# Performance work log

Measured on AMD Instinct MI355X. Metric: run time of the kernel, lower is better.

Reference implementation:

```python
import jax, jax.numpy as jnp
import numpy as np

B, D, N = 512, 512, 196  # batch, hidden dim, kb elements (14x14 feature grid)


def setup_inputs() -> dict:
    key = jax.random.key(0)
    ks = jax.random.split(key, 8)
    s = 1.0 / np.sqrt(D)
    return {
        "memory_state": jax.random.normal(ks[0], (B, D), jnp.float32),
        "knowledge_base": jax.random.normal(ks[1], (B, D, N), jnp.float32),
        "ctrl_state": jax.random.normal(ks[2], (B, D), jnp.float32),
        "kb_proj": jax.random.normal(ks[3], (B, D, N), jnp.float32),
        "W_mem": jax.random.normal(ks[4], (D, D), jnp.float32) * s,
        "b_mem": jnp.zeros((D,), jnp.float32),
        "W_cat": jax.random.normal(ks[5], (D, 2 * D), jnp.float32) * s,
        "b_cat": jnp.zeros((D,), jnp.float32),
        "W_attn": jax.random.normal(ks[6], (1, D), jnp.float32) * s,
        "b_attn": jnp.zeros((1,), jnp.float32),
    }


def reference(memory_state, knowledge_base, ctrl_state, kb_proj,
              W_mem, b_mem, W_cat, b_cat, W_attn, b_attn):
    # mem projection: [B, D]
    mem = memory_state @ W_mem.T + b_mem
    # interaction with projected knowledge base: [B, D, N]
    I_elements = mem[:, :, None] * kb_proj
    # concat along channel dim -> [B, 2D, N], permute to [B, N, 2D]
    cat = jnp.concatenate([I_elements, knowledge_base], axis=1).transpose(0, 2, 1)
    # concat layer: [B, N, D]
    concat = cat @ W_cat.T + b_cat
    # gate by control state, attention logits: [B, N]
    rai = ((concat * ctrl_state[:, None, :]) @ W_attn.T + b_attn)[:, :, 0]
    rvi = jax.nn.softmax(rai, axis=1)  # [B, N]
    # weighted sum over kb elements: [B, D]
    read_vector = jnp.einsum('bn,bdn->bd', rvi, knowledge_base)
    return read_vector
```

## Files before the change

kernel.cpp:

```cpp
#include <hip/hip_runtime.h>
#include <hip/hip_bf16.h>


constexpr int D = 512;
constexpr int N = 196;
constexpr int NF4 = 49;

using f4 = __attribute__((ext_vector_type(4))) float;

__global__ __launch_bounds__(256) void phase_a(
    const float* __restrict__ ms, const float* __restrict__ ctrl,
    const float* __restrict__ Wmem, const float* __restrict__ bmem,
    const float* __restrict__ Wcat, const float* __restrict__ Wattn,
    float* __restrict__ mem_ws, float* __restrict__ v_ws)
{
    constexpr int PAD = 68;
    __shared__ float As[16 * PAD];
    __shared__ float Bs[16 * PAD];

    const int bid = blockIdx.x;
    const int t   = threadIdx.x;
    const int tx  = t & 15, ty = t >> 4;

    const bool g1 = (bid < 64);
    int tile_m, tile_n;
    if (g1) { tile_m = (bid >> 3) * 64; tile_n = (bid & 7) * 64; }
    else    { int bb = bid - 64; tile_m = (bb >> 4) * 64; tile_n = (bb & 15) * 64; }

    float acc[4][4] = {};

    for (int k0 = 0; k0 < 512; k0 += 16) {
        {
            const int k = t & 15;
            const int mbase = t >> 4;
#pragma unroll
            for (int r = 0; r < 4; r++) {
                const int m = mbase + 16 * r;
                const int row = tile_m + m;
                float a;
                if (g1) a = ms[row * 512 + k0 + k];
                else    a = ctrl[row * 512 + k0 + k] * Wattn[k0 + k];
                As[k * PAD + m] = a;
            }
        }
        if (g1) {
            const int k = t & 15;
            const int nbase = t >> 4;
#pragma unroll
            for (int r = 0; r < 4; r++) {
                const int n = nbase + 16 * r;
                Bs[k * PAD + n] = Wmem[(tile_n + n) * 512 + k0 + k];
            }
        } else {
            const int n = t & 63;
            const int kbase = t >> 6;
#pragma unroll
            for (int r = 0; r < 4; r++) {
                const int k = kbase + 4 * r;
                Bs[k * PAD + n] = Wcat[(k0 + k) * 1024 + tile_n + n];
            }
        }
        __syncthreads();
#pragma unroll
        for (int k = 0; k < 16; k++) {
            const float4 av = *reinterpret_cast<const float4*>(&As[k * PAD + ty * 4]);
            const float4 bv = *reinterpret_cast<const float4*>(&Bs[k * PAD + tx * 4]);
            const float a[4] = {av.x, av.y, av.z, av.w};
            const float bb[4] = {bv.x, bv.y, bv.z, bv.w};
#pragma unroll
            for (int i = 0; i < 4; i++)
#pragma unroll
                for (int j = 0; j < 4; j++)
                    acc[i][j] += a[i] * bb[j];
        }
        __syncthreads();
    }

    if (g1) {
#pragma unroll
        for (int i = 0; i < 4; i++) {
            const int row = tile_m + ty * 4 + i;
#pragma unroll
            for (int j = 0; j < 4; j++) {
                const int col = tile_n + tx * 4 + j;
                mem_ws[row * 512 + col] = acc[i][j] + bmem[col];
            }
        }
    } else {
#pragma unroll
        for (int i = 0; i < 4; i++) {
            const int row = tile_m + ty * 4 + i;
#pragma unroll
            for (int j = 0; j < 4; j++) {
                const int col = tile_n + tx * 4 + j;
                v_ws[row * 1024 + col] = acc[i][j];
            }
        }
    }
}

__global__ __launch_bounds__(256) void k_rai(
    const f4* __restrict__ kb, const f4* __restrict__ kbp,
    const float* __restrict__ mem_ws, const float* __restrict__ v_ws,
    float* __restrict__ rai_ws)
{
    __shared__ float p_s[256];
    __shared__ float q_s[256];
    __shared__ float part[4][200];

    const int bid = blockIdx.x;
    const int b   = bid >> 1;
    const int s   = bid & 1;
    const int d0  = s * 256;
    const int t    = threadIdx.x;
    const int lane = t & 63;
    const int w    = t >> 6;

    {
        const int d = d0 + t;
        p_s[t] = mem_ws[b * D + d] * v_ws[b * 2 * D + d];
        q_s[t] = v_ws[b * 2 * D + D + d];
    }
    __syncthreads();

    const int lc = (lane < NF4) ? lane : (NF4 - 1);
    const f4* kb_b  = kb  + (size_t)b * (D * NF4);
    const f4* kbp_b = kbp + (size_t)b * (D * NF4);

    float a0 = 0.f, a1 = 0.f, a2 = 0.f, a3 = 0.f;
    const int dw = d0 + w * 64;
#pragma unroll 4
    for (int r = 0; r < 64; r++) {
        const int d = dw + r;
        const f4 vp = __builtin_nontemporal_load(&kbp_b[(size_t)d * NF4 + lc]);
        const f4 vk = kb_b[(size_t)d * NF4 + lc];
        const float pd = p_s[d - d0];
        const float qd = q_s[d - d0];
        a0 += pd * vp.x + qd * vk.x;
        a1 += pd * vp.y + qd * vk.y;
        a2 += pd * vp.z + qd * vk.z;
        a3 += pd * vp.w + qd * vk.w;
    }

    if (lane < NF4) {
        part[w][4 * lane + 0] = a0;
        part[w][4 * lane + 1] = a1;
        part[w][4 * lane + 2] = a2;
        part[w][4 * lane + 3] = a3;
    }
    __syncthreads();

    if (t < N) {
        const float r = part[0][t] + part[1][t] + part[2][t] + part[3][t];
        rai_ws[(size_t)(b * 2 + s) * N + t] = r;
    }
}

__global__ __launch_bounds__(256) void k_out(
    const f4* __restrict__ kb, const float* __restrict__ rai_ws,
    float* __restrict__ out)
{
    __shared__ float w_s[N];
    __shared__ float red[4];
    __shared__ float out_s[D];

    const int b    = 511 - (int)blockIdx.x;
    const int t    = threadIdx.x;
    const int lane = t & 63;
    const int w    = t >> 6;

    float e = 0.f;
    if (t < N) {
        const float r = rai_ws[(size_t)(b * 2) * N + t]
                      + rai_ws[(size_t)(b * 2 + 1) * N + t];
        e = __expf(r);
        w_s[t] = e;
    }
    float ssum = e;
#pragma unroll
    for (int m = 32; m; m >>= 1) ssum += __shfl_xor(ssum, m, 64);
    if (lane == 0) red[w] = ssum;
    __syncthreads();

    const float inv = 1.0f / (red[0] + red[1] + red[2] + red[3]);

    f4 wv = {0.f, 0.f, 0.f, 0.f};
    if (lane < NF4) {
        wv.x = w_s[4 * lane + 0] * inv;
        wv.y = w_s[4 * lane + 1] * inv;
        wv.z = w_s[4 * lane + 2] * inv;
        wv.w = w_s[4 * lane + 3] * inv;
    }

    const int lc = (lane < NF4) ? lane : (NF4 - 1);
    const f4* kb_b = kb + (size_t)b * (D * NF4);
    const int dw = w * 128;
#pragma unroll 4
    for (int r = 0; r < 128; r++) {
        const int d = dw + r;
        const f4 v = kb_b[(size_t)d * NF4 + lc];
        float sc = v.x * wv.x + v.y * wv.y + v.z * wv.z + v.w * wv.w;
#pragma unroll
        for (int m = 32; m; m >>= 1) sc += __shfl_xor(sc, m, 64);
        if (lane == 0) out_s[d] = sc;
    }
    __syncthreads();

    out[(size_t)b * D + t]       = out_s[t];
    out[(size_t)b * D + 256 + t] = out_s[256 + t];
}

extern "C" void kernel_launch(void* const* d_in, const int* in_sizes, int n_in,
                              void* d_out, int out_size, void* d_ws, size_t ws_size,
                              hipStream_t stream) {
    const float* ms    = (const float*)d_in[0];
    const float* kb    = (const float*)d_in[1];
    const float* ctrl  = (const float*)d_in[2];
    const float* kbp   = (const float*)d_in[3];
    const float* Wmem  = (const float*)d_in[4];
    const float* bmem  = (const float*)d_in[5];
    const float* Wcat  = (const float*)d_in[6];
    const float* Wattn = (const float*)d_in[8];

    float* mem_ws = (float*)d_ws;
    float* v_ws   = mem_ws + 512 * 512;
    float* rai_ws = v_ws + 512 * 1024;

    phase_a<<<192, 256, 0, stream>>>(ms, ctrl, Wmem, bmem, Wcat, Wattn, mem_ws, v_ws);
    k_rai<<<1024, 256, 0, stream>>>((const f4*)kb, (const f4*)kbp, mem_ws, v_ws, rai_ws);
    k_out<<<512, 256, 0, stream>>>((const f4*)kb, rai_ws, (float*)d_out);
}
```

Baseline: 546.0 us.

## Fuse logit and softmax-weighted-sum kernels into one per-batch 1024-thread block

Merges the attention-logit kernel and the softmax/weighted-sum kernel into a single kernel with one 1024-thread block per batch row. Each of 16 waves covers 32 hidden rows, and the block reduces partial logits in shared memory. The kb slice it just read is then re-read for the weighted sum while it may still sit in cache. This removes the rai workspace round trip and one launch. In exchange the grid drops from 1024 blocks to 512 larger ones, and a __launch_bounds__(1024, 8) hint may constrain registers.

```diff
diff --git a/kernel.cpp b/kernel.cpp
--- a/kernel.cpp
+++ b/kernel.cpp
@@ -99,27 +99,26 @@
     }
 }
 
-__global__ __launch_bounds__(256) void k_rai(
+__global__ __launch_bounds__(1024, 8) void k_fused(
     const f4* __restrict__ kb, const f4* __restrict__ kbp,
     const float* __restrict__ mem_ws, const float* __restrict__ v_ws,
-    float* __restrict__ rai_ws)
+    float* __restrict__ out)
 {
-    __shared__ float p_s[256];
-    __shared__ float q_s[256];
-    __shared__ float part[4][200];
-
-    const int bid = blockIdx.x;
-    const int b   = bid >> 1;
-    const int s   = bid & 1;
-    const int d0  = s * 256;
+    __shared__ float p_s[D];
+    __shared__ float q_s[D];
+    __shared__ float part[16][200];
+    __shared__ float w_s[200];
+    __shared__ float red[16];
+    __shared__ float out_s[D];
+
+    const int b    = blockIdx.x;
     const int t    = threadIdx.x;
     const int lane = t & 63;
     const int w    = t >> 6;
 
-    {
-        const int d = d0 + t;
-        p_s[t] = mem_ws[b * D + d] * v_ws[b * 2 * D + d];
-        q_s[t] = v_ws[b * 2 * D + D + d];
+    if (t < D) {
+        p_s[t] = mem_ws[b * D + t] * v_ws[b * 2 * D + t];
+        q_s[t] = v_ws[b * 2 * D + D + t];
     }
     __syncthreads();
 
@@ -128,14 +127,14 @@
     const f4* kbp_b = kbp + (size_t)b * (D * NF4);
 
     float a0 = 0.f, a1 = 0.f, a2 = 0.f, a3 = 0.f;
-    const int dw = d0 + w * 64;
+    const int dw = w * 32;
 #pragma unroll 4
-    for (int r = 0; r < 64; r++) {
+    for (int r = 0; r < 32; r++) {
         const int d = dw + r;
         const f4 vp = __builtin_nontemporal_load(&kbp_b[(size_t)d * NF4 + lc]);
         const f4 vk = kb_b[(size_t)d * NF4 + lc];
-        const float pd = p_s[d - d0];
-        const float qd = q_s[d - d0];
+        const float pd = p_s[d];
+        const float qd = q_s[d];
         a0 += pd * vp.x + qd * vk.x;
         a1 += pd * vp.y + qd * vk.y;
         a2 += pd * vp.z + qd * vk.z;
@@ -150,29 +149,11 @@
     }
     __syncthreads();
 
-    if (t < N) {
-        const float r = part[0][t] + part[1][t] + part[2][t] + part[3][t];
-        rai_ws[(size_t)(b * 2 + s) * N + t] = r;
-    }
-}
-
-__global__ __launch_bounds__(256) void k_out(
-    const f4* __restrict__ kb, const float* __restrict__ rai_ws,
-    float* __restrict__ out)
-{
-    __shared__ float w_s[N];
-    __shared__ float red[4];
-    __shared__ float out_s[D];
-
-    const int b    = 511 - (int)blockIdx.x;
-    const int t    = threadIdx.x;
-    const int lane = t & 63;
-    const int w    = t >> 6;
-
     float e = 0.f;
     if (t < N) {
-        const float r = rai_ws[(size_t)(b * 2) * N + t]
-                      + rai_ws[(size_t)(b * 2 + 1) * N + t];
+        float r = 0.f;
+#pragma unroll
+        for (int i = 0; i < 16; i++) r += part[i][t];
         e = __expf(r);
         w_s[t] = e;
     }
@@ -182,7 +163,10 @@
     if (lane == 0) red[w] = ssum;
     __syncthreads();
 
-    const float inv = 1.0f / (red[0] + red[1] + red[2] + red[3]);
+    float tot = 0.f;
+#pragma unroll
+    for (int i = 0; i < 16; i++) tot += red[i];
+    const float inv = 1.0f / tot;
 
     f4 wv = {0.f, 0.f, 0.f, 0.f};
     if (lane < NF4) {
@@ -192,11 +176,8 @@
         wv.w = w_s[4 * lane + 3] * inv;
     }
 
-    const int lc = (lane < NF4) ? lane : (NF4 - 1);
-    const f4* kb_b = kb + (size_t)b * (D * NF4);
-    const int dw = w * 128;
 #pragma unroll 4
-    for (int r = 0; r < 128; r++) {
+    for (int r = 0; r < 32; r++) {
         const int d = dw + r;
         const f4 v = kb_b[(size_t)d * NF4 + lc];
         float sc = v.x * wv.x + v.y * wv.y + v.z * wv.z + v.w * wv.w;
@@ -206,8 +187,7 @@
     }
     __syncthreads();
 
-    out[(size_t)b * D + t]       = out_s[t];
-    out[(size_t)b * D + 256 + t] = out_s[256 + t];
+    if (t < D) out[(size_t)b * D + t] = out_s[t];
 }
 
 extern "C" void kernel_launch(void* const* d_in, const int* in_sizes, int n_in,
@@ -224,9 +204,8 @@
 
     float* mem_ws = (float*)d_ws;
     float* v_ws   = mem_ws + 512 * 512;
-    float* rai_ws = v_ws + 512 * 1024;
 
     phase_a<<<192, 256, 0, stream>>>(ms, ctrl, Wmem, bmem, Wcat, Wattn, mem_ws, v_ws);
-    k_rai<<<1024, 256, 0, stream>>>((const f4*)kb, (const f4*)kbp, mem_ws, v_ws, rai_ws);
-    k_out<<<512, 256, 0, stream>>>((const f4*)kb, rai_ws, (float*)d_out);
+    k_fused<<<512, 1024, 0, stream>>>((const f4*)kb, (const f4*)kbp, mem_ws, v_ws,
+                                      (float*)d_out);
 }
```

Result: faster. 507.3 us (-7.1%).
